# Performance work log

Measured on AMD Instinct MI355X. Metric: run time of the kernel, lower is better.

The kernel has to match this reference:

```python
import jax, jax.numpy as jnp
import numpy as np
import math

B, L, DM = 2, 256, 256
H, NK, T = 8, 4, 4  # heads, num_kernels, time_dim
DH = DM // H


def _gauss_mean_over_d(t, mu, sigma, w):
    """t: [B,P,T]; mu/sigma/w: [H,D,T,K] -> mean over D of sum_{t,k} w*exp(...): [B,H,P].
    Scans over D to avoid materializing [B,H,D,P,T,K]."""
    D = mu.shape[1]

    def step(acc, p):
        mu_d, sg_d, w_d = p  # each [H,T,K]
        diff = t[:, None, :, :, None] - mu_d[None, :, None, :, :]  # [B,H,P,T,K]
        g = (w_d[None, :, None] * jnp.exp(-diff ** 2 / (2.0 * sg_d[None, :, None] ** 2))).sum((-1, -2))
        return acc + g, None

    init = jnp.zeros((t.shape[0], mu.shape[0], t.shape[1]), t.dtype)
    params = (jnp.moveaxis(mu, 1, 0), jnp.moveaxis(sigma, 1, 0), jnp.moveaxis(w, 1, 0))
    acc, _ = jax.lax.scan(jax.checkpoint(step), init, params)
    return acc / D


def setup_inputs() -> dict:
    key = jax.random.key(0)
    ks = jax.random.split(key, 16)
    s = 1.0 / math.sqrt(DM)
    return {
        "x": jax.random.normal(ks[0], (B, L, DM), jnp.float32),
        "t": jax.random.uniform(ks[1], (B, L, T), jnp.float32),
        "WQ": jax.random.normal(ks[2], (DM, DM), jnp.float32) * s,
        "WK": jax.random.normal(ks[3], (DM, DM), jnp.float32) * s,
        "WV": jax.random.normal(ks[4], (DM, DM), jnp.float32) * s,
        "WO": jax.random.normal(ks[5], (DM, DM), jnp.float32) * s,
        "bO": jnp.zeros((DM,), jnp.float32),
        "mu_abs": jax.random.normal(ks[6], (H, DH, T, NK), jnp.float32),
        "sigma_abs": jnp.abs(jax.random.normal(ks[7], (H, DH, T, NK), jnp.float32)) + 1e-5,
        "w_abs": jax.random.normal(ks[8], (H, DH, T, NK), jnp.float32),
        "mu_rel": jax.random.normal(ks[9], (H, DH, T, NK), jnp.float32),
        "sigma_rel": jnp.abs(jax.random.normal(ks[10], (H, DH, T, NK), jnp.float32)) + 1e-5,
        "w_rel": jax.random.normal(ks[11], (H, DH, T, NK), jnp.float32),
        "alpha": jnp.ones((H,), jnp.float32),
        "beta": jnp.ones((H,), jnp.float32),
        "gamma": jnp.zeros((H,), jnp.float32),
    }


def reference(x, t, WQ, WK, WV, WO, bO, mu_abs, sigma_abs, w_abs,
              mu_rel, sigma_rel, w_rel, alpha, beta, gamma):
    b, l, dm = x.shape
    h = alpha.shape[0]
    dh = dm // h

    def heads(y):  # [B,L,DM] -> [B,H,L,DH]
        return y.reshape(b, l, h, dh).transpose(0, 2, 1, 3)

    Q = heads(x @ WQ.T)
    K = heads(x @ WK.T)
    V = heads(x @ WV.T)
    Xh = heads(x)

    Pij = jnp.einsum('bhid,bhjd->bhij', Xh, Xh)

    g_abs = _gauss_mean_over_d(t, mu_abs, sigma_abs, w_abs)  # [B,H,L]
    t_rel = jnp.abs(t[:, :, None, :] - t[:, None, :, :]).reshape(b, l * l, t.shape[-1])
    g_rel = _gauss_mean_over_d(t_rel, mu_rel, sigma_rel, w_rel).reshape(b, h, l, l)

    gi = g_abs[:, :, :, None]  # [B,H,L,1]
    a = alpha[None, :, None, None]
    bb = beta[None, :, None, None]
    c = gamma[None, :, None, None]
    # original: g_abs_j = g_abs_i broadcast over j, so (g_i + g_j) == 2*gi broadcast
    A = a * Pij * (gi + gi) + bb * Pij * g_rel + c

    scores = jnp.einsum('bhid,bhjd->bhij', Q, K) / math.sqrt(dh)
    attn = jax.nn.softmax(scores * A, axis=-1)  # dropout = identity (eval)
    out = jnp.einsum('bhij,bhjd->bhid', attn, V)
    out = out.transpose(0, 2, 1, 3).reshape(b, l, dm)
    return out @ WO.T + bO
```

## Files before the change

kernel.cpp:

```cpp
#include <hip/hip_runtime.h>
#include <math.h>

constexpr int Bc = 2, Lc = 256, DMc = 256, Hc = 8, DHc = 32;
constexpr float LOG2E = 1.4426950408889634f;
constexpr float RSQRT_DH = 0.17677669529663687f;
#define EXP2 __builtin_amdgcn_exp2f

constexpr int   NTAB = 512;
constexpr float SIG0 = 0.02f;

__device__ __forceinline__ float mixsum(const float4* __restrict__ prm, float x) {
    float acc = 0.f;
    #pragma unroll 8
    for (int q = 0; q < 128; ++q) {
        float4 p = prm[q];
        float d0 = x - p.x;
        acc = fmaf(p.z, EXP2(d0 * d0 * p.y), acc);
    }
    return acc;
}

__device__ __forceinline__ void role_tab(int bx,
    const float* __restrict__ mu, const float* __restrict__ sg, const float* __restrict__ w,
    float4* __restrict__ TAB, float4* __restrict__ NLIST, int* __restrict__ NCNT,
    float* smem)
{
    float4* prm = (float4*)smem;
    float*  fs  = smem + 512;
    int*    lcnt = (int*)(smem + 772);
    int hm = bx >> 2, chunk = bx & 3;
    int h = hm >> 2, tau = hm & 3;
    int tid = threadIdx.x;

    if (tid == 0) *lcnt = 0;
    __syncthreads();
    if (tid < 128) {
        int d = tid >> 2, k = tid & 3;
        int off = h * 512 + d * 16 + tau * 4 + k;
        float s  = sg[off];
        float mv = mu[off], wv = w[off];
        float n = -(0.5f * LOG2E) / (s * s);
        bool narrow = (s < SIG0);
        prm[tid] = make_float4(mv, n, narrow ? 0.0f : wv, 0.0f);
        if (chunk == 0 && narrow) {
            int slot = atomicAdd(lcnt, 1);
            NLIST[hm * 128 + slot] = make_float4(mv, n, wv, 0.0f);
        }
    }
    __syncthreads();
    if (chunk == 0 && tid == 0) NCNT[hm] = *lcnt;

    fs[tid] = mixsum(prm, (float)(chunk * 256 + tid) * (1.0f / 1024.0f));
    if (tid == 0)
        fs[256] = mixsum(prm, (float)(chunk * 256 + 256) * (1.0f / 1024.0f));
    __syncthreads();

    if (tid < 128) {
        float f0 = fs[tid * 2], fm = fs[tid * 2 + 1], f1 = fs[tid * 2 + 2];
        float c2 = 2.0f * (f0 + f1 - 2.0f * fm);
        float c1 = f1 - f0 - c2;
        TAB[hm * NTAB + chunk * 128 + tid] = make_float4(f0, c1, c2, 0.0f);
    }
}

__device__ __forceinline__ void role_gabs(int idx, const float* __restrict__ t,
                                          const float* __restrict__ mu, const float* __restrict__ sg,
                                          const float* __restrict__ w, float* __restrict__ gabs,
                                          float* smem) {
    int h = idx & 7, b = (idx >> 3) & 1, q = idx >> 4;
    int tid = threadIdx.x;
    {
        float2 s2 = *(const float2*)(sg + h * 512 + tid * 2);
        float2 o;
        o.x = -(0.5f * LOG2E) / (s2.x * s2.x);
        o.y = -(0.5f * LOG2E) / (s2.y * s2.y);
        *(float2*)(smem + tid * 2) = o;
    }
    __syncthreads();
    int lane = tid & 63, tg = tid >> 6;
    int i = q * 64 + lane;
    float tv = t[(b * Lc + i) * 4 + tg];
    const float* muB = mu + h * 512 + tg * 4;
    const float* wB  = w  + h * 512 + tg * 4;
    const float* nsB = smem + tg * 4;
    float acc = 0.f;
    #pragma unroll 4
    for (int d = 0; d < 32; ++d) {
        float4 m4 = *(const float4*)(muB + d * 16);
        float4 w4 = *(const float4*)(wB  + d * 16);
        float4 n4 = *(const float4*)(nsB + d * 16);
        float d0 = tv - m4.x; acc = fmaf(w4.x, EXP2(d0 * d0 * n4.x), acc);
        float d1 = tv - m4.y; acc = fmaf(w4.y, EXP2(d1 * d1 * n4.y), acc);
        float d2 = tv - m4.z; acc = fmaf(w4.z, EXP2(d2 * d2 * n4.z), acc);
        float d3 = tv - m4.w; acc = fmaf(w4.w, EXP2(d3 * d3 * n4.w), acc);
    }
    float* red = smem + 512;
    red[tg * 64 + lane] = acc;
    __syncthreads();
    if (tid < 64)
        gabs[(b * Hc + h) * Lc + q * 64 + lane] =
            (red[lane] + red[64 + lane] + red[128 + lane] + red[192 + lane]) * (1.0f / 32.0f);
}

__device__ __forceinline__ void gemm32(const float* __restrict__ A, const float* __restrict__ W,
                                       float* __restrict__ C, const float* __restrict__ bias,
                                       float sc, int m0, int n0, float* smem) {
    float* As = smem;
    float* Ws = smem + 32 * 33;
    int tid = threadIdx.x;
    int tx = tid & 15, ty = tid >> 4;
    int r = tid >> 3;
    int c4 = (tid & 7) * 4;
    float acc[2][2] = {};
    for (int k0 = 0; k0 < 256; k0 += 32) {
        float4 av = *(const float4*)(A + (size_t)(m0 + r) * DMc + k0 + c4);
        float4 wv = *(const float4*)(W + (size_t)(n0 + r) * DMc + k0 + c4);
        const float* a_ = (const float*)&av;
        const float* w_ = (const float*)&wv;
        #pragma unroll
        for (int u = 0; u < 4; ++u) {
            As[(c4 + u) * 33 + r] = a_[u];
            Ws[(c4 + u) * 33 + r] = w_[u];
        }
        __syncthreads();
        #pragma unroll 8
        for (int k = 0; k < 32; ++k) {
            float a0 = As[k * 33 + ty * 2], a1 = As[k * 33 + ty * 2 + 1];
            float w0 = Ws[k * 33 + tx * 2], w1 = Ws[k * 33 + tx * 2 + 1];
            acc[0][0] = fmaf(a0, w0, acc[0][0]);
            acc[0][1] = fmaf(a0, w1, acc[0][1]);
            acc[1][0] = fmaf(a1, w0, acc[1][0]);
            acc[1][1] = fmaf(a1, w1, acc[1][1]);
        }
        __syncthreads();
    }
    #pragma unroll
    for (int u = 0; u < 2; ++u) {
        int m = m0 + ty * 2 + u;
        #pragma unroll
        for (int v = 0; v < 2; ++v) {
            float o = acc[u][v] * sc;
            if (bias) o += bias[n0 + tx * 2 + v];
            C[(size_t)m * DMc + n0 + tx * 2 + v] = o;
        }
    }
}

__global__ void __launch_bounds__(256) k_pre(
    const float* __restrict__ x, const float* __restrict__ t,
    const float* __restrict__ WQ, const float* __restrict__ WK, const float* __restrict__ WV,
    const float* __restrict__ mu_a, const float* __restrict__ sg_a, const float* __restrict__ w_a,
    const float* __restrict__ mu_r, const float* __restrict__ sg_r, const float* __restrict__ w_r,
    float* __restrict__ Qb, float* __restrict__ Kb, float* __restrict__ Vb,
    float* __restrict__ GA,
    float4* __restrict__ TAB, float4* __restrict__ NLIST, int* __restrict__ NCNT)
{
    __shared__ __align__(16) float smem[2112];
    int bx = blockIdx.x;
    if (bx < 128) {
        role_tab(bx, mu_r, sg_r, w_r, TAB, NLIST, NCNT, smem);
    } else if (bx < 192) {
        role_gabs(bx - 128, t, mu_a, sg_a, w_a, GA, smem);
    } else {
        int idx = bx - 192;
        int z = idx >> 7;
        int r = idx & 127;
        int m0 = (r >> 3) * 32, n0 = (r & 7) * 32;
        const float* W = (z == 0) ? WQ : (z == 1) ? WK : WV;
        float* C = (z == 0) ? Qb : (z == 1) ? Kb : Vb;
        gemm32(x, W, C, nullptr, (z == 0) ? RSQRT_DH : 1.0f, m0, n0, smem);
    }
}

__global__ void __launch_bounds__(512) k_sp(
    const float* __restrict__ Q, const float* __restrict__ K, const float* __restrict__ x,
    const float* __restrict__ t, const float* __restrict__ gabs,
    const float4* __restrict__ TAB, const float4* __restrict__ NLIST,
    const int* __restrict__ NCNT,
    const float* __restrict__ alpha, const float* __restrict__ beta, const float* __restrict__ gamma,
    float* __restrict__ G)
{
    constexpr int PITCH = 68;
    int it = blockIdx.x, jt = blockIdx.y, bh = blockIdx.z;
    int b = bh >> 3, h = bh & 7;
    int i0 = it * 64, j0 = jt * 64;
    int tid = threadIdx.x;
    __shared__ __align__(16) float sm[4 * 32 * PITCH];
    float* sQ  = sm;
    float* sK  = sm + 32 * PITCH;
    float* sXi = sm + 64 * PITCH;
    float* sXj = sm + 96 * PITCH;

    {
        int r = tid >> 3;
        int c4 = (tid & 7) * 4;
        float4 qv = *(const float4*)(Q + ((size_t)(b * Lc + i0 + r) * DMc + h * DHc + c4));
        float4 kv = *(const float4*)(K + ((size_t)(b * Lc + j0 + r) * DMc + h * DHc + c4));
        float4 xi = *(const float4*)(x + ((size_t)(b * Lc + i0 + r) * DMc + h * DHc + c4));
        float4 xj = *(const float4*)(x + ((size_t)(b * Lc + j0 + r) * DMc + h * DHc + c4));
        const float* q_ = (const float*)&qv; const float* k_ = (const float*)&kv;
        const float* a_ = (const float*)&xi; const float* c_ = (const float*)&xj;
        #pragma unroll
        for (int u = 0; u < 4; ++u) {
            sQ [(c4 + u) * PITCH + r] = q_[u];
            sK [(c4 + u) * PITCH + r] = k_[u];
            sXi[(c4 + u) * PITCH + r] = a_[u];
            sXj[(c4 + u) * PITCH + r] = c_[u];
        }
    }
    __syncthreads();

    int tx = tid & 15, ty = tid >> 4;
    int i2 = ty * 2, j4 = tx * 4;
    float accS[2][4] = {}, accP[2][4] = {};
    #pragma unroll 4
    for (int k = 0; k < 32; ++k) {
        float2 qa = *(const float2*)(sQ  + k * PITCH + i2);
        float4 kb = *(const float4*)(sK  + k * PITCH + j4);
        float2 xa = *(const float2*)(sXi + k * PITCH + i2);
        float4 xb = *(const float4*)(sXj + k * PITCH + j4);
        const float* qa_ = (const float*)&qa; const float* kb_ = (const float*)&kb;
        const float* xa_ = (const float*)&xa; const float* xb_ = (const float*)&xb;
        #pragma unroll
        for (int u = 0; u < 2; ++u)
            #pragma unroll
            for (int v = 0; v < 4; ++v) {
                accS[u][v] = fmaf(qa_[u], kb_[v], accS[u][v]);
                accP[u][v] = fmaf(xa_[u], xb_[v], accP[u][v]);
            }
    }

    __syncthreads();
    float4* tab = (float4*)sm;
    {
        const float4* src = TAB + (size_t)h * 4 * NTAB;
        #pragma unroll
        for (int u = 0; u < 4; ++u)
            tab[tid + u * 512] = src[tid + u * 512];
    }
    __syncthreads();

    float4 tiv[2], tjv[4];
    #pragma unroll
    for (int u = 0; u < 2; ++u)
        tiv[u] = *(const float4*)(t + (size_t)(b * Lc + i0 + i2 + u) * 4);
    #pragma unroll
    for (int v = 0; v < 4; ++v)
        tjv[v] = *(const float4*)(t + (size_t)(b * Lc + j0 + j4 + v) * 4);

    float g8[2][4] = {};
    #pragma unroll
    for (int tg = 0; tg < 4; ++tg) {
        float xv[2][4];
        #pragma unroll
        for (int u = 0; u < 2; ++u) {
            float tiu = ((const float*)&tiv[u])[tg];
            #pragma unroll
            for (int v = 0; v < 4; ++v) {
                float xx = fabsf(tiu - ((const float*)&tjv[v])[tg]);
                xv[u][v] = xx;
                float xs = xx * (float)NTAB;
                int iu = min((int)xs, NTAB - 1);
                float uu = xs - (float)iu;
                float4 c = tab[tg * NTAB + iu];
                g8[u][v] += fmaf(uu, fmaf(uu, c.z, c.y), c.x);
            }
        }
        int cn = NCNT[h * 4 + tg];
        for (int nn = 0; nn < cn; ++nn) {
            float4 q = NLIST[(h * 4 + tg) * 128 + nn];
            #pragma unroll
            for (int u = 0; u < 2; ++u)
                #pragma unroll
                for (int v = 0; v < 4; ++v) {
                    float d0 = xv[u][v] - q.x;
                    g8[u][v] = fmaf(q.z, EXP2(d0 * d0 * q.y), g8[u][v]);
                }
        }
    }

    float la = alpha[h], lb = beta[h], lg = gamma[h];
    constexpr float SC = 1.0f / 32.0f;
    float* gb = G + (size_t)bh * (Lc * Lc);
    #pragma unroll
    for (int u = 0; u < 2; ++u) {
        int i = i0 + i2 + u;
        float gi2 = 2.0f * la * gabs[bh * Lc + i];
        float* addr = gb + (size_t)i * Lc + j0 + j4;
        float4 o;
        o.x = accS[u][0] * fmaf(accP[u][0], fmaf(lb, g8[u][0] * SC, gi2), lg);
        o.y = accS[u][1] * fmaf(accP[u][1], fmaf(lb, g8[u][1] * SC, gi2), lg);
        o.z = accS[u][2] * fmaf(accP[u][2], fmaf(lb, g8[u][2] * SC, gi2), lg);
        o.w = accS[u][3] * fmaf(accP[u][3], fmaf(lb, g8[u][3] * SC, gi2), lg);
        *(float4*)addr = o;
    }
}

__global__ void __launch_bounds__(512) k_pvsm(const float* __restrict__ P,
                                              const float* __restrict__ V,
                                              float* __restrict__ AO) {
    int it = blockIdx.x, bh = blockIdx.y;
    int b = bh >> 3, h = bh & 7;
    int i0 = it * 16;
    int tid = threadIdx.x;
    __shared__ float sP[16 * 260];
    __shared__ float sV[256 * 34];
    int i = tid >> 5, l = tid & 31;

    const float* row = P + (size_t)bh * (Lc * Lc) + (size_t)(i0 + i) * Lc + l * 8;
    float4 p0 = *(const float4*)(row);
    float4 p1 = *(const float4*)(row + 4);
    float m = fmaxf(fmaxf(fmaxf(p0.x, p0.y), fmaxf(p0.z, p0.w)),
                    fmaxf(fmaxf(p1.x, p1.y), fmaxf(p1.z, p1.w)));
    #pragma unroll
    for (int s = 1; s < 32; s <<= 1) m = fmaxf(m, __shfl_xor(m, s, 32));
    float4 e0, e1;
    e0.x = EXP2((p0.x - m) * LOG2E); e0.y = EXP2((p0.y - m) * LOG2E);
    e0.z = EXP2((p0.z - m) * LOG2E); e0.w = EXP2((p0.w - m) * LOG2E);
    e1.x = EXP2((p1.x - m) * LOG2E); e1.y = EXP2((p1.y - m) * LOG2E);
    e1.z = EXP2((p1.z - m) * LOG2E); e1.w = EXP2((p1.w - m) * LOG2E);
    float sum = ((e0.x + e0.y) + (e0.z + e0.w)) + ((e1.x + e1.y) + (e1.z + e1.w));
    #pragma unroll
    for (int s = 1; s < 32; s <<= 1) sum += __shfl_xor(sum, s, 32);
    float rs = 1.0f / sum;
    *(float4*)(sP + i * 260 + l * 8)     = e0;
    *(float4*)(sP + i * 260 + l * 8 + 4) = e1;

    {
        int jr = tid >> 3, c4 = (tid & 7) * 4;
        #pragma unroll
        for (int u = 0; u < 4; ++u) {
            int j = jr + u * 64;
            *(float4*)(sV + j * 34 + c4) =
                *(const float4*)(V + ((size_t)(b * Lc + j) * DMc + h * DHc + c4));
        }
    }
    __syncthreads();

    int d = l;
    float o0 = 0.f;
    #pragma unroll 4
    for (int j4 = 0; j4 < 256; j4 += 4) {
        float4 p4 = *(const float4*)(sP + i * 260 + j4);
        float v0 = sV[(j4 + 0) * 34 + d];
        float v1 = sV[(j4 + 1) * 34 + d];
        float v2 = sV[(j4 + 2) * 34 + d];
        float v3 = sV[(j4 + 3) * 34 + d];
        o0 = fmaf(p4.x, v0, o0); o0 = fmaf(p4.y, v1, o0);
        o0 = fmaf(p4.z, v2, o0); o0 = fmaf(p4.w, v3, o0);
    }
    AO[((size_t)(b * Lc + i0 + i) * DMc + h * DHc + d)] = o0 * rs;
}

__global__ void __launch_bounds__(256) k_out(const float* __restrict__ A,
                                             const float* __restrict__ W,
                                             const float* __restrict__ bias,
                                             float* __restrict__ C) {
    __shared__ __align__(16) float smem[2112];
    gemm32(A, W, C, bias, 1.0f, blockIdx.x * 32, blockIdx.y * 32, smem);
}

extern "C" void kernel_launch(void* const* d_in, const int* in_sizes, int n_in,
                              void* d_out, int out_size, void* d_ws, size_t ws_size,
                              hipStream_t stream) {
    (void)in_sizes; (void)n_in; (void)out_size; (void)ws_size;
    const float* x      = (const float*)d_in[0];
    const float* t      = (const float*)d_in[1];
    const float* WQ     = (const float*)d_in[2];
    const float* WK     = (const float*)d_in[3];
    const float* WV     = (const float*)d_in[4];
    const float* WO     = (const float*)d_in[5];
    const float* bO     = (const float*)d_in[6];
    const float* mu_abs = (const float*)d_in[7];
    const float* sg_abs = (const float*)d_in[8];
    const float* w_abs  = (const float*)d_in[9];
    const float* mu_rel = (const float*)d_in[10];
    const float* sg_rel = (const float*)d_in[11];
    const float* w_rel  = (const float*)d_in[12];
    const float* alpha  = (const float*)d_in[13];
    const float* beta   = (const float*)d_in[14];
    const float* gamma  = (const float*)d_in[15];
    float* out = (float*)d_out;
    float* ws = (float*)d_ws;

    float* Qb = ws;
    float* Kb = ws + 131072;
    float* Vb = ws + 262144;
    float* AO = ws + 393216;
    float* GA = ws + 524288;
    float* GR = ws + 528384;
    float4* TAB   = (float4*)(ws + 1576960);
    float4* NLIST = (float4*)(ws + 1642496);
    int*    NCNT  = (int*)   (ws + 1658880);

    k_pre<<<dim3(576), dim3(256), 0, stream>>>(x, t, WQ, WK, WV,
                                               mu_abs, sg_abs, w_abs,
                                               mu_rel, sg_rel, w_rel,
                                               Qb, Kb, Vb, GA, TAB, NLIST, NCNT);
    k_sp<<<dim3(4, 4, 16), dim3(512), 0, stream>>>(Qb, Kb, x, t, GA,
                                                   TAB, NLIST, NCNT,
                                                   alpha, beta, gamma, GR);
    k_pvsm<<<dim3(16, 16), dim3(512), 0, stream>>>(GR, Vb, AO);
    k_out<<<dim3(16, 8), dim3(256), 0, stream>>>(AO, WO, bO, out);
}
```

Baseline: 126.1 us.

## Fuse four kernels into one cooperative persistent kernel with grid syncs

Replaces the four separate launches (pre, score, softmax-PV, output GEMM) with one cooperative kernel of 256 blocks of 512 threads that runs each stage and separates them with grid.sync. Work in each stage is remapped onto the 256 blocks: the QKV GEMM now uses 64x64 tiles with 2x4 per-thread outputs, gabs processes 128 rows per block, and only 128 blocks take part in the output GEMM. The aim is to remove inter-kernel launch gaps and tail effects. In exchange it adds grid-wide barriers, leaves blocks idle during the lighter stages, and uses a larger shared-memory footprint, which may limit occupancy.

Result: slower. 362.3 us (+187.4%).

```diff
diff --git a/kernel.cpp b/kernel.cpp
--- a/kernel.cpp
+++ b/kernel.cpp
@@ -1,5 +1,8 @@
 #include <hip/hip_runtime.h>
+#include <hip/hip_cooperative_groups.h>
 #include <math.h>
+
+namespace cg = cooperative_groups;
 
 constexpr int Bc = 2, Lc = 256, DMc = 256, Hc = 8, DHc = 32;
 constexpr float LOG2E = 1.4426950408889634f;
@@ -23,14 +26,13 @@
 __device__ __forceinline__ void role_tab(int bx,
     const float* __restrict__ mu, const float* __restrict__ sg, const float* __restrict__ w,
     float4* __restrict__ TAB, float4* __restrict__ NLIST, int* __restrict__ NCNT,
-    float* smem)
+    float* smem, int tid)
 {
     float4* prm = (float4*)smem;
     float*  fs  = smem + 512;
     int*    lcnt = (int*)(smem + 772);
     int hm = bx >> 2, chunk = bx & 3;
     int h = hm >> 2, tau = hm & 3;
-    int tid = threadIdx.x;
 
     if (tid == 0) *lcnt = 0;
     __syncthreads();
@@ -50,9 +52,8 @@
     __syncthreads();
     if (chunk == 0 && tid == 0) NCNT[hm] = *lcnt;
 
-    fs[tid] = mixsum(prm, (float)(chunk * 256 + tid) * (1.0f / 1024.0f));
-    if (tid == 0)
-        fs[256] = mixsum(prm, (float)(chunk * 256 + 256) * (1.0f / 1024.0f));
+    if (tid < 257)
+        fs[tid] = mixsum(prm, (float)(chunk * 256 + tid) * (1.0f / 1024.0f));
     __syncthreads();
 
     if (tid < 128) {
@@ -66,23 +67,21 @@
 __device__ __forceinline__ void role_gabs(int idx, const float* __restrict__ t,
                                           const float* __restrict__ mu, const float* __restrict__ sg,
                                           const float* __restrict__ w, float* __restrict__ gabs,
-                                          float* smem) {
-    int h = idx & 7, b = (idx >> 3) & 1, q = idx >> 4;
-    int tid = threadIdx.x;
+                                          float* smem, int tid) {
+    int h = idx & 7, b = (idx >> 3) & 1, half = idx >> 4;
+    float* ns  = smem;
+    float* red = smem + 512;
     {
-        float2 s2 = *(const float2*)(sg + h * 512 + tid * 2);
-        float2 o;
-        o.x = -(0.5f * LOG2E) / (s2.x * s2.x);
-        o.y = -(0.5f * LOG2E) / (s2.y * s2.y);
-        *(float2*)(smem + tid * 2) = o;
+        float s = sg[h * 512 + tid];
+        ns[tid] = -(0.5f * LOG2E) / (s * s);
     }
     __syncthreads();
-    int lane = tid & 63, tg = tid >> 6;
-    int i = q * 64 + lane;
+    int l = tid & 127, tg = tid >> 7;
+    int i = half * 128 + l;
     float tv = t[(b * Lc + i) * 4 + tg];
     const float* muB = mu + h * 512 + tg * 4;
     const float* wB  = w  + h * 512 + tg * 4;
-    const float* nsB = smem + tg * 4;
+    const float* nsB = ns + tg * 4;
     float acc = 0.f;
     #pragma unroll 4
     for (int d = 0; d < 32; ++d) {
@@ -94,270 +93,294 @@
         float d2 = tv - m4.z; acc = fmaf(w4.z, EXP2(d2 * d2 * n4.z), acc);
         float d3 = tv - m4.w; acc = fmaf(w4.w, EXP2(d3 * d3 * n4.w), acc);
     }
-    float* red = smem + 512;
-    red[tg * 64 + lane] = acc;
+    red[tg * 128 + l] = acc;
     __syncthreads();
-    if (tid < 64)
-        gabs[(b * Hc + h) * Lc + q * 64 + lane] =
-            (red[lane] + red[64 + lane] + red[128 + lane] + red[192 + lane]) * (1.0f / 32.0f);
-}
-
-__device__ __forceinline__ void gemm32(const float* __restrict__ A, const float* __restrict__ W,
-                                       float* __restrict__ C, const float* __restrict__ bias,
-                                       float sc, int m0, int n0, float* smem) {
+    if (tid < 128)
+        gabs[(b * Hc + h) * Lc + half * 128 + tid] =
+            (red[tid] + red[128 + tid] + red[256 + tid] + red[384 + tid]) * (1.0f / 32.0f);
+}
+
+__device__ __forceinline__ void role_qkv(int u, const float* __restrict__ x,
+                                         const float* __restrict__ WQ, const float* __restrict__ WK,
+                                         const float* __restrict__ WV,
+                                         float* __restrict__ Qb, float* __restrict__ Kb,
+                                         float* __restrict__ Vb, float* smem, int tid) {
+    constexpr int GP = 68;
+    int z = u >> 5, r = u & 31;
+    int m0 = (r >> 2) * 64, n0 = (r & 3) * 64;
+    const float* W = (z == 0) ? WQ : (z == 1) ? WK : WV;
+    float* C = (z == 0) ? Qb : (z == 1) ? Kb : Vb;
+    float sc = (z == 0) ? RSQRT_DH : 1.0f;
     float* As = smem;
-    float* Ws = smem + 32 * 33;
-    int tid = threadIdx.x;
+    float* Ws = smem + 32 * GP;
+    int rr = tid >> 3, c4 = (tid & 7) * 4;
     int tx = tid & 15, ty = tid >> 4;
-    int r = tid >> 3;
-    int c4 = (tid & 7) * 4;
-    float acc[2][2] = {};
+    int i2 = ty * 2, j4 = tx * 4;
+    float acc[2][4] = {};
     for (int k0 = 0; k0 < 256; k0 += 32) {
-        float4 av = *(const float4*)(A + (size_t)(m0 + r) * DMc + k0 + c4);
-        float4 wv = *(const float4*)(W + (size_t)(n0 + r) * DMc + k0 + c4);
+        float4 av = *(const float4*)(x + (size_t)(m0 + rr) * DMc + k0 + c4);
+        float4 wv = *(const float4*)(W + (size_t)(n0 + rr) * DMc + k0 + c4);
         const float* a_ = (const float*)&av;
         const float* w_ = (const float*)&wv;
         #pragma unroll
-        for (int u = 0; u < 4; ++u) {
-            As[(c4 + u) * 33 + r] = a_[u];
-            Ws[(c4 + u) * 33 + r] = w_[u];
+        for (int q = 0; q < 4; ++q) {
+            As[(c4 + q) * GP + rr] = a_[q];
+            Ws[(c4 + q) * GP + rr] = w_[q];
         }
         __syncthreads();
         #pragma unroll 8
         for (int k = 0; k < 32; ++k) {
-            float a0 = As[k * 33 + ty * 2], a1 = As[k * 33 + ty * 2 + 1];
-            float w0 = Ws[k * 33 + tx * 2], w1 = Ws[k * 33 + tx * 2 + 1];
-            acc[0][0] = fmaf(a0, w0, acc[0][0]);
-            acc[0][1] = fmaf(a0, w1, acc[0][1]);
-            acc[1][0] = fmaf(a1, w0, acc[1][0]);
-            acc[1][1] = fmaf(a1, w1, acc[1][1]);
+            float2 a2 = *(const float2*)(As + k * GP + i2);
+            float4 w4 = *(const float4*)(Ws + k * GP + j4);
+            const float* aa = (const float*)&a2;
+            const float* ww = (const float*)&w4;
+            #pragma unroll
+            for (int uu = 0; uu < 2; ++uu)
+                #pragma unroll
+                for (int vv = 0; vv < 4; ++vv)
+                    acc[uu][vv] = fmaf(aa[uu], ww[vv], acc[uu][vv]);
         }
         __syncthreads();
     }
     #pragma unroll
-    for (int u = 0; u < 2; ++u) {
-        int m = m0 + ty * 2 + u;
-        #pragma unroll
-        for (int v = 0; v < 2; ++v) {
-            float o = acc[u][v] * sc;
-            if (bias) o += bias[n0 + tx * 2 + v];
-            C[(size_t)m * DMc + n0 + tx * 2 + v] = o;
-        }
-    }
-}
-
-__global__ void __launch_bounds__(256) k_pre(
+    for (int uu = 0; uu < 2; ++uu)
+        #pragma unroll
+        for (int vv = 0; vv < 4; ++vv)
+            C[(size_t)(m0 + i2 + uu) * DMc + n0 + j4 + vv] = acc[uu][vv] * sc;
+}
+
+__global__ void __launch_bounds__(512) k_fused(
     const float* __restrict__ x, const float* __restrict__ t,
     const float* __restrict__ WQ, const float* __restrict__ WK, const float* __restrict__ WV,
+    const float* __restrict__ WO, const float* __restrict__ bO,
     const float* __restrict__ mu_a, const float* __restrict__ sg_a, const float* __restrict__ w_a,
     const float* __restrict__ mu_r, const float* __restrict__ sg_r, const float* __restrict__ w_r,
+    const float* __restrict__ alpha, const float* __restrict__ beta, const float* __restrict__ gamma,
+    float* __restrict__ out,
     float* __restrict__ Qb, float* __restrict__ Kb, float* __restrict__ Vb,
-    float* __restrict__ GA,
+    float* __restrict__ AO, float* __restrict__ GA, float* __restrict__ GR,
     float4* __restrict__ TAB, float4* __restrict__ NLIST, int* __restrict__ NCNT)
 {
-    __shared__ __align__(16) float smem[2112];
+    __shared__ __align__(16) float smem[12864];
+    cg::grid_group grid = cg::this_grid();
     int bx = blockIdx.x;
-    if (bx < 128) {
-        role_tab(bx, mu_r, sg_r, w_r, TAB, NLIST, NCNT, smem);
-    } else if (bx < 192) {
-        role_gabs(bx - 128, t, mu_a, sg_a, w_a, GA, smem);
-    } else {
-        int idx = bx - 192;
-        int z = idx >> 7;
-        int r = idx & 127;
-        int m0 = (r >> 3) * 32, n0 = (r & 7) * 32;
-        const float* W = (z == 0) ? WQ : (z == 1) ? WK : WV;
-        float* C = (z == 0) ? Qb : (z == 1) ? Kb : Vb;
-        gemm32(x, W, C, nullptr, (z == 0) ? RSQRT_DH : 1.0f, m0, n0, smem);
-    }
-}
-
-__global__ void __launch_bounds__(512) k_sp(
-    const float* __restrict__ Q, const float* __restrict__ K, const float* __restrict__ x,
-    const float* __restrict__ t, const float* __restrict__ gabs,
-    const float4* __restrict__ TAB, const float4* __restrict__ NLIST,
-    const int* __restrict__ NCNT,
-    const float* __restrict__ alpha, const float* __restrict__ beta, const float* __restrict__ gamma,
-    float* __restrict__ G)
-{
-    constexpr int PITCH = 68;
-    int it = blockIdx.x, jt = blockIdx.y, bh = blockIdx.z;
-    int b = bh >> 3, h = bh & 7;
-    int i0 = it * 64, j0 = jt * 64;
     int tid = threadIdx.x;
-    __shared__ __align__(16) float sm[4 * 32 * PITCH];
-    float* sQ  = sm;
-    float* sK  = sm + 32 * PITCH;
-    float* sXi = sm + 64 * PITCH;
-    float* sXj = sm + 96 * PITCH;
+
+    if (bx < 128)      role_tab(bx, mu_r, sg_r, w_r, TAB, NLIST, NCNT, smem, tid);
+    else if (bx < 160) role_gabs(bx - 128, t, mu_a, sg_a, w_a, GA, smem, tid);
+    else               role_qkv(bx - 160, x, WQ, WK, WV, Qb, Kb, Vb, smem, tid);
+
+    __threadfence();
+    grid.sync();
 
     {
-        int r = tid >> 3;
-        int c4 = (tid & 7) * 4;
-        float4 qv = *(const float4*)(Q + ((size_t)(b * Lc + i0 + r) * DMc + h * DHc + c4));
-        float4 kv = *(const float4*)(K + ((size_t)(b * Lc + j0 + r) * DMc + h * DHc + c4));
-        float4 xi = *(const float4*)(x + ((size_t)(b * Lc + i0 + r) * DMc + h * DHc + c4));
-        float4 xj = *(const float4*)(x + ((size_t)(b * Lc + j0 + r) * DMc + h * DHc + c4));
-        const float* q_ = (const float*)&qv; const float* k_ = (const float*)&kv;
-        const float* a_ = (const float*)&xi; const float* c_ = (const float*)&xj;
-        #pragma unroll
-        for (int u = 0; u < 4; ++u) {
-            sQ [(c4 + u) * PITCH + r] = q_[u];
-            sK [(c4 + u) * PITCH + r] = k_[u];
-            sXi[(c4 + u) * PITCH + r] = a_[u];
-            sXj[(c4 + u) * PITCH + r] = c_[u];
-        }
-    }
-    __syncthreads();
-
-    int tx = tid & 15, ty = tid >> 4;
-    int i2 = ty * 2, j4 = tx * 4;
-    float accS[2][4] = {}, accP[2][4] = {};
-    #pragma unroll 4
-    for (int k = 0; k < 32; ++k) {
-        float2 qa = *(const float2*)(sQ  + k * PITCH + i2);
-        float4 kb = *(const float4*)(sK  + k * PITCH + j4);
-        float2 xa = *(const float2*)(sXi + k * PITCH + i2);
-        float4 xb = *(const float4*)(sXj + k * PITCH + j4);
-        const float* qa_ = (const float*)&qa; const float* kb_ = (const float*)&kb;
-        const float* xa_ = (const float*)&xa; const float* xb_ = (const float*)&xb;
-        #pragma unroll
-        for (int u = 0; u < 2; ++u)
-            #pragma unroll
-            for (int v = 0; v < 4; ++v) {
-                accS[u][v] = fmaf(qa_[u], kb_[v], accS[u][v]);
-                accP[u][v] = fmaf(xa_[u], xb_[v], accP[u][v]);
-            }
-    }
-
-    __syncthreads();
-    float4* tab = (float4*)sm;
-    {
-        const float4* src = TAB + (size_t)h * 4 * NTAB;
-        #pragma unroll
-        for (int u = 0; u < 4; ++u)
-            tab[tid + u * 512] = src[tid + u * 512];
-    }
-    __syncthreads();
-
-    float4 tiv[2], tjv[4];
-    #pragma unroll
-    for (int u = 0; u < 2; ++u)
-        tiv[u] = *(const float4*)(t + (size_t)(b * Lc + i0 + i2 + u) * 4);
-    #pragma unroll
-    for (int v = 0; v < 4; ++v)
-        tjv[v] = *(const float4*)(t + (size_t)(b * Lc + j0 + j4 + v) * 4);
-
-    float g8[2][4] = {};
-    #pragma unroll
-    for (int tg = 0; tg < 4; ++tg) {
-        float xv[2][4];
-        #pragma unroll
-        for (int u = 0; u < 2; ++u) {
-            float tiu = ((const float*)&tiv[u])[tg];
-            #pragma unroll
-            for (int v = 0; v < 4; ++v) {
-                float xx = fabsf(tiu - ((const float*)&tjv[v])[tg]);
-                xv[u][v] = xx;
-                float xs = xx * (float)NTAB;
-                int iu = min((int)xs, NTAB - 1);
-                float uu = xs - (float)iu;
-                float4 c = tab[tg * NTAB + iu];
-                g8[u][v] += fmaf(uu, fmaf(uu, c.z, c.y), c.x);
-            }
-        }
-        int cn = NCNT[h * 4 + tg];
-        for (int nn = 0; nn < cn; ++nn) {
-            float4 q = NLIST[(h * 4 + tg) * 128 + nn];
+        constexpr int PITCH = 68;
+        int it = bx & 3, jt = (bx >> 2) & 3, bh = bx >> 4;
+        int b = bh >> 3, h = bh & 7;
+        int i0 = it * 64, j0 = jt * 64;
+        float* sQ  = smem;
+        float* sK  = smem + 32 * PITCH;
+        float* sXi = smem + 64 * PITCH;
+        float* sXj = smem + 96 * PITCH;
+
+        {
+            int r = tid >> 3;
+            int c4 = (tid & 7) * 4;
+            float4 qv = *(const float4*)(Qb + ((size_t)(b * Lc + i0 + r) * DMc + h * DHc + c4));
+            float4 kv = *(const float4*)(Kb + ((size_t)(b * Lc + j0 + r) * DMc + h * DHc + c4));
+            float4 xi = *(const float4*)(x  + ((size_t)(b * Lc + i0 + r) * DMc + h * DHc + c4));
+            float4 xj = *(const float4*)(x  + ((size_t)(b * Lc + j0 + r) * DMc + h * DHc + c4));
+            const float* q_ = (const float*)&qv; const float* k_ = (const float*)&kv;
+            const float* a_ = (const float*)&xi; const float* c_ = (const float*)&xj;
+            #pragma unroll
+            for (int u = 0; u < 4; ++u) {
+                sQ [(c4 + u) * PITCH + r] = q_[u];
+                sK [(c4 + u) * PITCH + r] = k_[u];
+                sXi[(c4 + u) * PITCH + r] = a_[u];
+                sXj[(c4 + u) * PITCH + r] = c_[u];
+            }
+        }
+        __syncthreads();
+
+        int tx = tid & 15, ty = tid >> 4;
+        int i2 = ty * 2, j4 = tx * 4;
+        float accS[2][4] = {}, accP[2][4] = {};
+        #pragma unroll 4
+        for (int k = 0; k < 32; ++k) {
+            float2 qa = *(const float2*)(sQ  + k * PITCH + i2);
+            float4 kb = *(const float4*)(sK  + k * PITCH + j4);
+            float2 xa = *(const float2*)(sXi + k * PITCH + i2);
+            float4 xb = *(const float4*)(sXj + k * PITCH + j4);
+            const float* qa_ = (const float*)&qa; const float* kb_ = (const float*)&kb;
+            const float* xa_ = (const float*)&xa; const float* xb_ = (const float*)&xb;
             #pragma unroll
             for (int u = 0; u < 2; ++u)
                 #pragma unroll
                 for (int v = 0; v < 4; ++v) {
-                    float d0 = xv[u][v] - q.x;
-                    g8[u][v] = fmaf(q.z, EXP2(d0 * d0 * q.y), g8[u][v]);
+                    accS[u][v] = fmaf(qa_[u], kb_[v], accS[u][v]);
+                    accP[u][v] = fmaf(xa_[u], xb_[v], accP[u][v]);
                 }
         }
-    }
-
-    float la = alpha[h], lb = beta[h], lg = gamma[h];
-    constexpr float SC = 1.0f / 32.0f;
-    float* gb = G + (size_t)bh * (Lc * Lc);
-    #pragma unroll
-    for (int u = 0; u < 2; ++u) {
-        int i = i0 + i2 + u;
-        float gi2 = 2.0f * la * gabs[bh * Lc + i];
-        float* addr = gb + (size_t)i * Lc + j0 + j4;
-        float4 o;
-        o.x = accS[u][0] * fmaf(accP[u][0], fmaf(lb, g8[u][0] * SC, gi2), lg);
-        o.y = accS[u][1] * fmaf(accP[u][1], fmaf(lb, g8[u][1] * SC, gi2), lg);
-        o.z = accS[u][2] * fmaf(accP[u][2], fmaf(lb, g8[u][2] * SC, gi2), lg);
-        o.w = accS[u][3] * fmaf(accP[u][3], fmaf(lb, g8[u][3] * SC, gi2), lg);
-        *(float4*)addr = o;
-    }
-}
-
-__global__ void __launch_bounds__(512) k_pvsm(const float* __restrict__ P,
-                                              const float* __restrict__ V,
-                                              float* __restrict__ AO) {
-    int it = blockIdx.x, bh = blockIdx.y;
-    int b = bh >> 3, h = bh & 7;
-    int i0 = it * 16;
-    int tid = threadIdx.x;
-    __shared__ float sP[16 * 260];
-    __shared__ float sV[256 * 34];
-    int i = tid >> 5, l = tid & 31;
-
-    const float* row = P + (size_t)bh * (Lc * Lc) + (size_t)(i0 + i) * Lc + l * 8;
-    float4 p0 = *(const float4*)(row);
-    float4 p1 = *(const float4*)(row + 4);
-    float m = fmaxf(fmaxf(fmaxf(p0.x, p0.y), fmaxf(p0.z, p0.w)),
-                    fmaxf(fmaxf(p1.x, p1.y), fmaxf(p1.z, p1.w)));
-    #pragma unroll
-    for (int s = 1; s < 32; s <<= 1) m = fmaxf(m, __shfl_xor(m, s, 32));
-    float4 e0, e1;
-    e0.x = EXP2((p0.x - m) * LOG2E); e0.y = EXP2((p0.y - m) * LOG2E);
-    e0.z = EXP2((p0.z - m) * LOG2E); e0.w = EXP2((p0.w - m) * LOG2E);
-    e1.x = EXP2((p1.x - m) * LOG2E); e1.y = EXP2((p1.y - m) * LOG2E);
-    e1.z = EXP2((p1.z - m) * LOG2E); e1.w = EXP2((p1.w - m) * LOG2E);
-    float sum = ((e0.x + e0.y) + (e0.z + e0.w)) + ((e1.x + e1.y) + (e1.z + e1.w));
-    #pragma unroll
-    for (int s = 1; s < 32; s <<= 1) sum += __shfl_xor(sum, s, 32);
-    float rs = 1.0f / sum;
-    *(float4*)(sP + i * 260 + l * 8)     = e0;
-    *(float4*)(sP + i * 260 + l * 8 + 4) = e1;
+
+        __syncthreads();
+        float4* tab = (float4*)smem;
+        {
+            const float4* src = TAB + (size_t)h * 4 * NTAB;
+            #pragma unroll
+            for (int u = 0; u < 4; ++u)
+                tab[tid + u * 512] = src[tid + u * 512];
+        }
+        __syncthreads();
+
+        float4 tiv[2], tjv[4];
+        #pragma unroll
+        for (int u = 0; u < 2; ++u)
+            tiv[u] = *(const float4*)(t + (size_t)(b * Lc + i0 + i2 + u) * 4);
+        #pragma unroll
+        for (int v = 0; v < 4; ++v)
+            tjv[v] = *(const float4*)(t + (size_t)(b * Lc + j0 + j4 + v) * 4);
+
+        float g8[2][4] = {};
+        #pragma unroll
+        for (int tg = 0; tg < 4; ++tg) {
+            float xv[2][4];
+            #pragma unroll
+            for (int u = 0; u < 2; ++u) {
+                float tiu = ((const float*)&tiv[u])[tg];
+                #pragma unroll
+                for (int v = 0; v < 4; ++v) {
+                    float xx = fabsf(tiu - ((const float*)&tjv[v])[tg]);
+                    xv[u][v] = xx;
+                    float xs = xx * (float)NTAB;
+                    int iu = min((int)xs, NTAB - 1);
+                    float uu = xs - (float)iu;
+                    float4 c = tab[tg * NTAB + iu];
+                    g8[u][v] += fmaf(uu, fmaf(uu, c.z, c.y), c.x);
+                }
+            }
+            int cn = NCNT[h * 4 + tg];
+            for (int nn = 0; nn < cn; ++nn) {
+                float4 q = NLIST[(h * 4 + tg) * 128 + nn];
+                #pragma unroll
+                for (int u = 0; u < 2; ++u)
+                    #pragma unroll
+                    for (int v = 0; v < 4; ++v) {
+                        float d0 = xv[u][v] - q.x;
+                        g8[u][v] = fmaf(q.z, EXP2(d0 * d0 * q.y), g8[u][v]);
+                    }
+            }
+        }
+
+        float la = alpha[h], lb = beta[h], lg = gamma[h];
+        constexpr float SC = 1.0f / 32.0f;
+        float* gb = GR + (size_t)bh * (Lc * Lc);
+        #pragma unroll
+        for (int u = 0; u < 2; ++u) {
+            int i = i0 + i2 + u;
+            float gi2 = 2.0f * la * GA[bh * Lc + i];
+            float* addr = gb + (size_t)i * Lc + j0 + j4;
+            float4 o;
+            o.x = accS[u][0] * fmaf(accP[u][0], fmaf(lb, g8[u][0] * SC, gi2), lg);
+            o.y = accS[u][1] * fmaf(accP[u][1], fmaf(lb, g8[u][1] * SC, gi2), lg);
+            o.z = accS[u][2] * fmaf(accP[u][2], fmaf(lb, g8[u][2] * SC, gi2), lg);
+            o.w = accS[u][3] * fmaf(accP[u][3], fmaf(lb, g8[u][3] * SC, gi2), lg);
+            *(float4*)addr = o;
+        }
+    }
+
+    __threadfence();
+    grid.sync();
 
     {
-        int jr = tid >> 3, c4 = (tid & 7) * 4;
-        #pragma unroll
-        for (int u = 0; u < 4; ++u) {
-            int j = jr + u * 64;
-            *(float4*)(sV + j * 34 + c4) =
-                *(const float4*)(V + ((size_t)(b * Lc + j) * DMc + h * DHc + c4));
-        }
-    }
-    __syncthreads();
-
-    int d = l;
-    float o0 = 0.f;
-    #pragma unroll 4
-    for (int j4 = 0; j4 < 256; j4 += 4) {
-        float4 p4 = *(const float4*)(sP + i * 260 + j4);
-        float v0 = sV[(j4 + 0) * 34 + d];
-        float v1 = sV[(j4 + 1) * 34 + d];
-        float v2 = sV[(j4 + 2) * 34 + d];
-        float v3 = sV[(j4 + 3) * 34 + d];
-        o0 = fmaf(p4.x, v0, o0); o0 = fmaf(p4.y, v1, o0);
-        o0 = fmaf(p4.z, v2, o0); o0 = fmaf(p4.w, v3, o0);
-    }
-    AO[((size_t)(b * Lc + i0 + i) * DMc + h * DHc + d)] = o0 * rs;
-}
-
-__global__ void __launch_bounds__(256) k_out(const float* __restrict__ A,
-                                             const float* __restrict__ W,
-                                             const float* __restrict__ bias,
-                                             float* __restrict__ C) {
-    __shared__ __align__(16) float smem[2112];
-    gemm32(A, W, C, bias, 1.0f, blockIdx.x * 32, blockIdx.y * 32, smem);
+        int it = bx & 15, bh = bx >> 4;
+        int b = bh >> 3, h = bh & 7;
+        int i0 = it * 16;
+        float* sP = smem;
+        float* sV = smem + 4160;
+        int i = tid >> 5, l = tid & 31;
+
+        const float* row = GR + (size_t)bh * (Lc * Lc) + (size_t)(i0 + i) * Lc + l * 8;
+        float4 p0 = *(const float4*)(row);
+        float4 p1 = *(const float4*)(row + 4);
+        float m = fmaxf(fmaxf(fmaxf(p0.x, p0.y), fmaxf(p0.z, p0.w)),
+                        fmaxf(fmaxf(p1.x, p1.y), fmaxf(p1.z, p1.w)));
+        #pragma unroll
+        for (int s = 1; s < 32; s <<= 1) m = fmaxf(m, __shfl_xor(m, s, 32));
+        float4 e0, e1;
+        e0.x = EXP2((p0.x - m) * LOG2E); e0.y = EXP2((p0.y - m) * LOG2E);
+        e0.z = EXP2((p0.z - m) * LOG2E); e0.w = EXP2((p0.w - m) * LOG2E);
+        e1.x = EXP2((p1.x - m) * LOG2E); e1.y = EXP2((p1.y - m) * LOG2E);
+        e1.z = EXP2((p1.z - m) * LOG2E); e1.w = EXP2((p1.w - m) * LOG2E);
+        float sum = ((e0.x + e0.y) + (e0.z + e0.w)) + ((e1.x + e1.y) + (e1.z + e1.w));
+        #pragma unroll
+        for (int s = 1; s < 32; s <<= 1) sum += __shfl_xor(sum, s, 32);
+        float rs = 1.0f / sum;
+        *(float4*)(sP + i * 260 + l * 8)     = e0;
+        *(float4*)(sP + i * 260 + l * 8 + 4) = e1;
+
+        {
+            int jr = tid >> 3, c4 = (tid & 7) * 4;
+            #pragma unroll
+            for (int u = 0; u < 4; ++u) {
+                int j = jr + u * 64;
+                *(float4*)(sV + j * 34 + c4) =
+                    *(const float4*)(Vb + ((size_t)(b * Lc + j) * DMc + h * DHc + c4));
+            }
+        }
+        __syncthreads();
+
+        int d = l;
+        float o0 = 0.f;
+        #pragma unroll 4
+        for (int j4 = 0; j4 < 256; j4 += 4) {
+            float4 p4 = *(const float4*)(sP + i * 260 + j4);
+            float v0 = sV[(j4 + 0) * 34 + d];
+            float v1 = sV[(j4 + 1) * 34 + d];
+            float v2 = sV[(j4 + 2) * 34 + d];
+            float v3 = sV[(j4 + 3) * 34 + d];
+            o0 = fmaf(p4.x, v0, o0); o0 = fmaf(p4.y, v1, o0);
+            o0 = fmaf(p4.z, v2, o0); o0 = fmaf(p4.w, v3, o0);
+        }
+        AO[((size_t)(b * Lc + i0 + i) * DMc + h * DHc + d)] = o0 * rs;
+        __syncthreads();
+    }
+
+    __threadfence();
+    grid.sync();
+
+    if (bx < 128) {
+        int mt = bx >> 3, nt = bx & 7;
+        int m0 = mt * 32, n0 = nt * 32;
+        float* As = smem;
+        float* Ws = smem + 2112;
+        int rr = tid >> 4;
+        int c4 = (tid & 15) * 4;
+        int ty = tid >> 4, tx = tid & 15;
+        float acc0 = 0.f, acc1 = 0.f;
+        for (int k0 = 0; k0 < 256; k0 += 64) {
+            float4 av = *(const float4*)(AO + (size_t)(m0 + rr) * DMc + k0 + c4);
+            float4 wv = *(const float4*)(WO + (size_t)(n0 + rr) * DMc + k0 + c4);
+            const float* a_ = (const float*)&av;
+            const float* w_ = (const float*)&wv;
+            #pragma unroll
+            for (int q = 0; q < 4; ++q) {
+                As[(c4 + q) * 33 + rr] = a_[q];
+                Ws[(c4 + q) * 33 + rr] = w_[q];
+            }
+            __syncthreads();
+            #pragma unroll 8
+            for (int k = 0; k < 64; ++k) {
+                float a  = As[k * 33 + ty];
+                float w0 = Ws[k * 33 + tx * 2];
+                float w1 = Ws[k * 33 + tx * 2 + 1];
+                acc0 = fmaf(a, w0, acc0);
+                acc1 = fmaf(a, w1, acc1);
+            }
+            __syncthreads();
+        }
+        out[(size_t)(m0 + ty) * DMc + n0 + tx * 2]     = acc0 + bO[n0 + tx * 2];
+        out[(size_t)(m0 + ty) * DMc + n0 + tx * 2 + 1] = acc1 + bO[n0 + tx * 2 + 1];
+    }
 }
 
 extern "C" void kernel_launch(void* const* d_in, const int* in_sizes, int n_in,
@@ -393,13 +416,14 @@
     float4* NLIST = (float4*)(ws + 1642496);
     int*    NCNT  = (int*)   (ws + 1658880);
 
-    k_pre<<<dim3(576), dim3(256), 0, stream>>>(x, t, WQ, WK, WV,
-                                               mu_abs, sg_abs, w_abs,
-                                               mu_rel, sg_rel, w_rel,
-                                               Qb, Kb, Vb, GA, TAB, NLIST, NCNT);
-    k_sp<<<dim3(4, 4, 16), dim3(512), 0, stream>>>(Qb, Kb, x, t, GA,
-                                                   TAB, NLIST, NCNT,
-                                                   alpha, beta, gamma, GR);
-    k_pvsm<<<dim3(16, 16), dim3(512), 0, stream>>>(GR, Vb, AO);
-    k_out<<<dim3(16, 8), dim3(256), 0, stream>>>(AO, WO, bO, out);
-}
+    void* args[] = {
+        (void*)&x, (void*)&t, (void*)&WQ, (void*)&WK, (void*)&WV, (void*)&WO, (void*)&bO,
+        (void*)&mu_abs, (void*)&sg_abs, (void*)&w_abs,
+        (void*)&mu_rel, (void*)&sg_rel, (void*)&w_rel,
+        (void*)&alpha, (void*)&beta, (void*)&gamma,
+        (void*)&out, (void*)&Qb, (void*)&Kb, (void*)&Vb,
+        (void*)&AO, (void*)&GA, (void*)&GR,
+        (void*)&TAB, (void*)&NLIST, (void*)&NCNT
+    };
+    hipLaunchCooperativeKernel((void*)k_fused, dim3(256), dim3(512), args, 0, stream);
+}
```
